# Kernel optimization log

Measured on AMD Instinct MI355X. Metric: run time of the kernel, lower is better.

Reference implementation:

```python
import jax, jax.numpy as jnp
import numpy as np

B, N, H, IN, OUT = 2, 4096, 64, 32, 8


def setup_inputs() -> dict:
    key = jax.random.key(0)
    ks = jax.random.split(key, 18)
    sc = 0.1  # xavier-ish scale for H=64
    mask = lambda k: (jax.random.uniform(k, (1, N, N)) < 0.1).astype(jnp.float32)
    return {
        "x0": jax.random.normal(ks[0], (B, N, IN), jnp.float32),
        "h0": jax.random.normal(ks[1], (B, N, H), jnp.float32),
        "h1": jax.random.normal(ks[2], (B, N, H), jnp.float32),
        "h2": jax.random.normal(ks[3], (B, N, H), jnp.float32),
        "m00": mask(ks[4]), "m20": mask(ks[5]), "m01": mask(ks[6]),
        "m11": mask(ks[7]), "m12": mask(ks[8]), "m22": mask(ks[9]),
        "Wq": jax.random.normal(ks[10], (3, H, H), jnp.float32) * sc,
        "Wk": jax.random.normal(ks[11], (6, H, H), jnp.float32) * sc,
        "Wsu0": jax.random.normal(ks[12], (H, IN + H), jnp.float32) * sc,
        "Wsu12": jax.random.normal(ks[13], (2, H, H), jnp.float32) * sc,
        "Wdt": jax.random.normal(ks[14], (3, H, H), jnp.float32) * sc,
        "bdt": jnp.zeros((3, H), jnp.float32),
        "step_size": jnp.array(1.0, jnp.float32),
        "out_scale": jnp.array(10.0, jnp.float32),
    }


def _cosine_acc(q, keys_and_masks_and_vals):
    # q: [B,N,H]; each entry: (keys [B,Np,H], mask [1,N,Np], vals [B,Np,H])
    qn = q / jnp.linalg.norm(q, axis=2, keepdims=True)
    acc = 0.0
    for k, m, v in keys_and_masks_and_vals:
        kn = k / jnp.linalg.norm(k, axis=2, keepdims=True)
        scale = 1.0 / jnp.sum(m, axis=2, keepdims=True)
        rel = scale * m * jnp.einsum("bnh,bmh->bnm", qn, kn)  # [B,N,Np]
        acc = acc + jnp.einsum("bnm,bmh->bnh", rel, v)
    return acc


def reference(x0, h0, h1, h2, m00, m20, m01, m11, m12, m22,
              Wq, Wk, Wsu0, Wsu12, Wdt, bdt, step_size, out_scale):
    # queries per successor type, keys per edge; edges (pred->succ):
    # 0->0 (k0), 2->0 (k1), 0->1 (k2), 1->1 (k3), 1->2 (k4), 2->2 (k5)
    q0 = h0 @ Wq[0].T
    q1 = h1 @ Wq[1].T
    q2 = h2 @ Wq[2].T
    acc0 = _cosine_acc(q0, [(h0 @ Wk[0].T, m00, h0), (h2 @ Wk[1].T, m20, h2)])
    acc1 = _cosine_acc(q1, [(h0 @ Wk[2].T, m01, h0), (h1 @ Wk[3].T, m11, h1)])
    acc2 = _cosine_acc(q2, [(h1 @ Wk[4].T, m12, h1), (h2 @ Wk[5].T, m22, h2)])

    def step(h, acc_in, Wsu, t):
        dt = 2.0 * jax.nn.sigmoid(h @ Wdt[t].T + bdt[t]) - 1.0
        return h + step_size * dt * (acc_in @ Wsu.T)

    h0n = step(h0, jnp.concatenate([x0, acc0], axis=2), Wsu0, 0)
    h1n = step(h1, acc1, Wsu12[0], 1)
    h2n = step(h2, acc2, Wsu12[1], 2)
    out2 = out_scale * h2n[:, :, :OUT]
    return (out2, h0n, h1n, h2n)
```

## Files before the change

kernel.cpp:

```cpp
#include <hip/hip_runtime.h>

typedef __bf16 bf16;
typedef bf16 bf16x8 __attribute__((ext_vector_type(8)));
typedef float f32x4 __attribute__((ext_vector_type(4)));
typedef unsigned int u32x4 __attribute__((ext_vector_type(4)));
typedef unsigned short u16x8 __attribute__((ext_vector_type(8)));
typedef unsigned int uint;

constexpr int NT = 4096;

__device__ __forceinline__ bf16x8 ld8f(const float* p) {
    f32x4 a = *(const f32x4*)p;
    f32x4 b = *(const f32x4*)(p + 4);
    bf16x8 v;
    v[0] = (bf16)a[0]; v[1] = (bf16)a[1]; v[2] = (bf16)a[2]; v[3] = (bf16)a[3];
    v[4] = (bf16)b[0]; v[5] = (bf16)b[1]; v[6] = (bf16)b[2]; v[7] = (bf16)b[3];
    return v;
}

__device__ __forceinline__ uint pack2(float a, float b) {
    unsigned short ua = __builtin_bit_cast(unsigned short, (bf16)a);
    unsigned short ub = __builtin_bit_cast(unsigned short, (bf16)b);
    return (uint)ua | ((uint)ub << 16);
}

__global__ __launch_bounds__(256) void prep_kernel(
    const float* __restrict__ h0, const float* __restrict__ h1, const float* __restrict__ h2,
    const float* __restrict__ Wq, const float* __restrict__ Wk,
    bf16* __restrict__ qn, bf16* __restrict__ kn, bf16* __restrict__ vT)
{
    __shared__ __align__(16) unsigned short tlds[4][16][72];
    const int tid = threadIdx.x, wid = tid >> 6, lane = tid & 63;
    const int l15 = lane & 15, quad = lane >> 4;
    const int bx = blockIdx.x;
    const int rt = bx & 127, sl = bx >> 7;
    const int g0 = rt * 64;
    const int grow = g0 + wid * 16 + l15;
    const float* hs[3] = {h0, h1, h2};

    bf16x8 af[3][2];
#pragma unroll
    for (int p = 0; p < 3; p++)
#pragma unroll
        for (int hc = 0; hc < 2; hc++)
            af[p][hc] = ld8f(hs[p] + (size_t)grow * 64 + hc * 32 + quad * 8);

    if (sl == 0) {
        const int gr0 = g0 + wid * 16;
        const int bb = gr0 >> 12, n0 = gr0 & 4095;
#pragma unroll
        for (int p = 0; p < 3; p++) {
#pragma unroll
            for (int hc = 0; hc < 2; hc++)
                *(u16x8*)(&tlds[wid][l15][hc * 32 + quad * 8]) = __builtin_bit_cast(u16x8, af[p][hc]);
            unsigned short vals[16];
#pragma unroll
            for (int r = 0; r < 16; r++) vals[r] = tlds[wid][r][lane];
            uint us[8];
#pragma unroll
            for (int k = 0; k < 8; k++) us[k] = (uint)vals[2 * k] | ((uint)vals[2 * k + 1] << 16);
            uint* dst = (uint*)(vT + ((size_t)(p * 2 + bb) * 64 + lane) * NT + n0);
            u32x4 w0 = {us[0], us[1], us[2], us[3]};
            u32x4 w1 = {us[4], us[5], us[6], us[7]};
            *(u32x4*)dst = w0;
            *(u32x4*)(dst + 4) = w1;
        }
    }

    const int predmap[6] = {0, 2, 0, 1, 1, 2};
    const int pj0 = sl * 3;
#pragma unroll
    for (int pi = 0; pi < 3; pi++) {
        const int pj = pj0 + pi;
        const float* W = (pj < 3) ? (Wq + pj * 4096) : (Wk + (pj - 3) * 4096);
        const int src = (pj < 3) ? pj : predmap[pj - 3];
        bf16* outp = (pj < 3) ? (qn + (size_t)pj * 2 * NT * 64)
                              : (kn + (size_t)(pj - 3) * 2 * NT * 64);
        f32x4 s[4];
#pragma unroll
        for (int it = 0; it < 4; it++) {
            f32x4 acc = {0.f, 0.f, 0.f, 0.f};
#pragma unroll
            for (int hc = 0; hc < 2; hc++) {
                bf16x8 wb = ld8f(W + (size_t)(it * 16 + l15) * 64 + hc * 32 + quad * 8);
                acc = __builtin_amdgcn_mfma_f32_16x16x32_bf16(af[src][hc], wb, acc, 0, 0, 0);
            }
            s[it] = acc;
        }
#pragma unroll
        for (int r = 0; r < 4; r++) {
            float ss = s[0][r] * s[0][r] + s[1][r] * s[1][r] + s[2][r] * s[2][r] + s[3][r] * s[3][r];
            ss += __shfl_xor(ss, 1); ss += __shfl_xor(ss, 2);
            ss += __shfl_xor(ss, 4); ss += __shfl_xor(ss, 8);
            float rn = rsqrtf(ss);
            s[0][r] *= rn; s[1][r] *= rn; s[2][r] *= rn; s[3][r] *= rn;
        }
        const int rowbase = g0 + wid * 16 + quad * 4;
#pragma unroll
        for (int it = 0; it < 4; it++)
#pragma unroll
            for (int r = 0; r < 4; r++)
                outp[(size_t)(rowbase + r) * 64 + it * 16 + l15] = (bf16)s[it][r];
    }
}

template<int JC>
__global__ __launch_bounds__(256, 3) void attn_kernel(
    const bf16* __restrict__ qn, const bf16* __restrict__ kn, const bf16* __restrict__ vT,
    const float* __restrict__ m00, const float* __restrict__ m20, const float* __restrict__ m01,
    const float* __restrict__ m11, const float* __restrict__ m12, const float* __restrict__ m22,
    float* __restrict__ Pacc, float* __restrict__ rsO)
{
    __shared__ __align__(16) bf16 Klds[2][64][72];
    __shared__ __align__(16) bf16 Vlds[2][64][72];
    const int tid = threadIdx.x, wid = tid >> 6, lane = tid & 63;
    const int l15 = lane & 15, quad = lane >> 4;
    const int bx = blockIdx.x;
    const int e = bx / (32 * JC);
    const int rem = bx % (32 * JC);
    const int qt = rem / JC, jcv = rem % JC;
    const int qrow0 = qt * 128, wstrip = wid * 32;
    const int qtypemap[6] = {0, 0, 1, 1, 2, 2};
    const int predmap[6]  = {0, 2, 0, 1, 1, 2};
    const float* masks[6] = {m00, m20, m01, m11, m12, m22};
    const float* __restrict__ mask = masks[e];
    const int qtv = qtypemap[e], pv = predmap[e];
    constexpr int JSPAN = NT / JC;
    const int jbeg = jcv * JSPAN, jend = jbeg + JSPAN;

    bf16x8 Qf[2][2][2];
#pragma unroll
    for (int b = 0; b < 2; b++)
#pragma unroll
        for (int mt = 0; mt < 2; mt++)
#pragma unroll
            for (int hc = 0; hc < 2; hc++)
                Qf[b][mt][hc] = *(const bf16x8*)(qn +
                    ((size_t)(qtv * 2 + b) * NT + qrow0 + wstrip + mt * 16 + l15) * 64 +
                    hc * 32 + quad * 8);

    f32x4 acc2[2][4][2];
#pragma unroll
    for (int b = 0; b < 2; b++)
#pragma unroll
        for (int ht = 0; ht < 4; ht++)
#pragma unroll
            for (int mt = 0; mt < 2; mt++) {
                f32x4 z = {0.f, 0.f, 0.f, 0.f};
                acc2[b][ht][mt] = z;
            }
    float rsl[2] = {0.f, 0.f};

#pragma unroll 1
    for (int j0 = jbeg; j0 < jend; j0 += 64) {
        __syncthreads();
#pragma unroll
        for (int i = 0; i < 4; i++) {
            int u = tid + 256 * i;
            int b = u >> 9, jl = (u >> 3) & 63, ch = u & 7;
            *(u32x4*)(&Klds[b][jl][ch * 8]) =
                *(const u32x4*)(kn + ((size_t)(e * 2 + b) * NT + j0 + jl) * 64 + ch * 8);
            *(u32x4*)(&Vlds[b][jl][ch * 8]) =
                *(const u32x4*)(vT + ((size_t)(pv * 2 + b) * 64 + jl) * NT + j0 + ch * 8);
        }
        __syncthreads();

        f32x4 mv[2][4];
#pragma unroll
        for (int mt = 0; mt < 2; mt++)
#pragma unroll
            for (int jt = 0; jt < 4; jt++) {
                mv[mt][jt] = *(const f32x4*)(mask +
                    (size_t)(qrow0 + wstrip + mt * 16 + l15) * NT + j0 + jt * 16 + quad * 4);
                rsl[mt] += mv[mt][jt][0] + mv[mt][jt][1] + mv[mt][jt][2] + mv[mt][jt][3];
            }

#pragma unroll
        for (int b = 0; b < 2; b++) {
            uint Pd[4][2][2];
#pragma unroll
            for (int jt = 0; jt < 4; jt++)
#pragma unroll
                for (int mt = 0; mt < 2; mt++) {
                    f32x4 sc = {0.f, 0.f, 0.f, 0.f};
#pragma unroll
                    for (int hc = 0; hc < 2; hc++) {
                        bf16x8 a = *(const bf16x8*)(&Klds[b][jt * 16 + l15][hc * 32 + quad * 8]);
                        sc = __builtin_amdgcn_mfma_f32_16x16x32_bf16(a, Qf[b][mt][hc], sc, 0, 0, 0);
                    }
                    sc[0] *= mv[mt][jt][0]; sc[1] *= mv[mt][jt][1];
                    sc[2] *= mv[mt][jt][2]; sc[3] *= mv[mt][jt][3];
                    Pd[jt][mt][0] = pack2(sc[0], sc[1]);
                    Pd[jt][mt][1] = pack2(sc[2], sc[3]);
                }

            uint Bf[2][2][4];
#pragma unroll
            for (int mt = 0; mt < 2; mt++)
#pragma unroll
                for (int c = 0; c < 2; c++)
#pragma unroll
                    for (int v = 0; v < 4; v++) {
                        int srclane = ((((quad & 1) * 2 + (v >> 1)) * 16 + l15) << 2);
                        int lo = __builtin_amdgcn_ds_bpermute(srclane, (int)Pd[2 * c][mt][v & 1]);
                        int hi = __builtin_amdgcn_ds_bpermute(srclane, (int)Pd[2 * c + 1][mt][v & 1]);
                        Bf[mt][c][v] = (quad & 2) ? (uint)hi : (uint)lo;
                    }

#pragma unroll
            for (int ht = 0; ht < 4; ht++)
#pragma unroll
                for (int c = 0; c < 2; c++) {
                    bf16x8 a = *(const bf16x8*)(&Vlds[b][ht * 16 + l15][c * 32 + quad * 8]);
#pragma unroll
                    for (int mt = 0; mt < 2; mt++) {
                        u32x4 t = {Bf[mt][c][0], Bf[mt][c][1], Bf[mt][c][2], Bf[mt][c][3]};
                        bf16x8 bbv = __builtin_bit_cast(bf16x8, t);
                        acc2[b][ht][mt] =
                            __builtin_amdgcn_mfma_f32_16x16x32_bf16(a, bbv, acc2[b][ht][mt], 0, 0, 0);
                    }
                }
        }
    }

#pragma unroll
    for (int b = 0; b < 2; b++)
#pragma unroll
        for (int ht = 0; ht < 4; ht++)
#pragma unroll
            for (int mt = 0; mt < 2; mt++) {
                int row = qrow0 + wstrip + mt * 16 + l15;
                *(f32x4*)(Pacc + (((size_t)(jcv * 6 + e) * 2 + b) * NT + row) * 64 +
                          ht * 16 + quad * 4) = acc2[b][ht][mt];
            }
#pragma unroll
    for (int mt = 0; mt < 2; mt++) {
        float v = rsl[mt];
        v += __shfl_xor(v, 16);
        v += __shfl_xor(v, 32);
        if (quad == 0)
            rsO[(size_t)(jcv * 6 + e) * NT + qrow0 + wstrip + mt * 16 + l15] = v;
    }
}

template<int JC>
__global__ __launch_bounds__(256) void update_kernel(
    const float* __restrict__ x0, const float* __restrict__ h0,
    const float* __restrict__ h1, const float* __restrict__ h2,
    const float* __restrict__ Wsu0, const float* __restrict__ Wsu12,
    const float* __restrict__ Wdt, const float* __restrict__ bdt,
    const float* __restrict__ stepp, const float* __restrict__ oscp,
    const float* __restrict__ Pacc, const float* __restrict__ rs,
    float* __restrict__ dout)
{
    const int tid = threadIdx.x, wid = tid >> 6, lane = tid & 63;
    const int l15 = lane & 15, quad = lane >> 4;
    const int bx = blockIdx.x;
    const int rt = bx & 127, t = bx >> 7;
    const int g0 = rt * 64;
    const int grow = g0 + wid * 16 + l15;
    const int n = grow & 4095, bb = grow >> 12;
    const float step = *stepp, osc = *oscp;
    const float* hs[3] = {h0, h1, h2};
    const float* __restrict__ ht_base = hs[t];

    bf16x8 afh[2], afacc[2], afx;
#pragma unroll
    for (int hc = 0; hc < 2; hc++)
        afh[hc] = ld8f(ht_base + (size_t)grow * 64 + hc * 32 + quad * 8);
    if (t == 0) afx = ld8f(x0 + (size_t)grow * 32 + quad * 8);

    float s0 = 0.f, s1 = 0.f;
#pragma unroll
    for (int jc = 0; jc < JC; jc++) {
        s0 += rs[(size_t)(jc * 6 + 2 * t) * NT + n];
        s1 += rs[(size_t)(jc * 6 + 2 * t + 1) * NT + n];
    }
    const float i0 = 1.f / s0, i1 = 1.f / s1;
#pragma unroll
    for (int hc = 0; hc < 2; hc++) {
        f32x4 A0 = {0.f,0.f,0.f,0.f}, A1 = {0.f,0.f,0.f,0.f};
        f32x4 B0 = {0.f,0.f,0.f,0.f}, B1 = {0.f,0.f,0.f,0.f};
#pragma unroll
        for (int jc = 0; jc < JC; jc++) {
            const float* p0 = Pacc + (((size_t)(jc * 6 + 2 * t) * 2 + bb) * NT + n) * 64 + hc * 32 + quad * 8;
            const float* p1 = Pacc + (((size_t)(jc * 6 + 2 * t + 1) * 2 + bb) * NT + n) * 64 + hc * 32 + quad * 8;
            A0 += *(const f32x4*)p0;       A1 += *(const f32x4*)(p0 + 4);
            B0 += *(const f32x4*)p1;       B1 += *(const f32x4*)(p1 + 4);
        }
        bf16x8 v;
        v[0] = (bf16)(A0[0] * i0 + B0[0] * i1);
        v[1] = (bf16)(A0[1] * i0 + B0[1] * i1);
        v[2] = (bf16)(A0[2] * i0 + B0[2] * i1);
        v[3] = (bf16)(A0[3] * i0 + B0[3] * i1);
        v[4] = (bf16)(A1[0] * i0 + B1[0] * i1);
        v[5] = (bf16)(A1[1] * i0 + B1[1] * i1);
        v[6] = (bf16)(A1[2] * i0 + B1[2] * i1);
        v[7] = (bf16)(A1[3] * i0 + B1[3] * i1);
        afacc[hc] = v;
    }

    float bdtv[4];
#pragma unroll
    for (int it = 0; it < 4; it++)
        bdtv[it] = bdt[t * 64 + it * 16 + l15];

#pragma unroll
    for (int it = 0; it < 4; it++) {
        f32x4 z = {0.f, 0.f, 0.f, 0.f};
        f32x4 u = {0.f, 0.f, 0.f, 0.f};
#pragma unroll
        for (int hc = 0; hc < 2; hc++) {
            bf16x8 wb = ld8f(Wdt + (size_t)t * 4096 + (size_t)(it * 16 + l15) * 64 + hc * 32 + quad * 8);
            z = __builtin_amdgcn_mfma_f32_16x16x32_bf16(afh[hc], wb, z, 0, 0, 0);
        }
        if (t == 0) {
            bf16x8 w0 = ld8f(Wsu0 + (size_t)(it * 16 + l15) * 96 + quad * 8);
            u = __builtin_amdgcn_mfma_f32_16x16x32_bf16(afx, w0, u, 0, 0, 0);
#pragma unroll
            for (int kc = 0; kc < 2; kc++) {
                bf16x8 wk = ld8f(Wsu0 + (size_t)(it * 16 + l15) * 96 + 32 + kc * 32 + quad * 8);
                u = __builtin_amdgcn_mfma_f32_16x16x32_bf16(afacc[kc], wk, u, 0, 0, 0);
            }
        } else {
#pragma unroll
            for (int kc = 0; kc < 2; kc++) {
                bf16x8 wk = ld8f(Wsu12 + (size_t)(t - 1) * 4096 + (size_t)(it * 16 + l15) * 64 + kc * 32 + quad * 8);
                u = __builtin_amdgcn_mfma_f32_16x16x32_bf16(afacc[kc], wk, u, 0, 0, 0);
            }
        }
        const int colg = it * 16 + l15;
#pragma unroll
        for (int r = 0; r < 4; r++) {
            int row = g0 + wid * 16 + quad * 4 + r;
            float zz = z[r] + bdtv[it];
            float dtv = 2.f / (1.f + __expf(-zz)) - 1.f;
            float hval = ht_base[(size_t)row * 64 + colg];
            float hn = hval + step * dtv * u[r];
            dout[65536 + (size_t)t * 524288 + (size_t)row * 64 + colg] = hn;
            if (t == 2 && colg < 8)
                dout[(size_t)row * 8 + colg] = osc * hn;
        }
    }
}

extern "C" void kernel_launch(void* const* d_in, const int* in_sizes, int n_in,
                              void* d_out, int out_size, void* d_ws, size_t ws_size,
                              hipStream_t stream) {
    const float* x0   = (const float*)d_in[0];
    const float* h0   = (const float*)d_in[1];
    const float* h1   = (const float*)d_in[2];
    const float* h2   = (const float*)d_in[3];
    const float* m00  = (const float*)d_in[4];
    const float* m20  = (const float*)d_in[5];
    const float* m01  = (const float*)d_in[6];
    const float* m11  = (const float*)d_in[7];
    const float* m12  = (const float*)d_in[8];
    const float* m22  = (const float*)d_in[9];
    const float* Wq   = (const float*)d_in[10];
    const float* Wk   = (const float*)d_in[11];
    const float* Wsu0 = (const float*)d_in[12];
    const float* Wsu12= (const float*)d_in[13];
    const float* Wdt  = (const float*)d_in[14];
    const float* bdt  = (const float*)d_in[15];
    const float* step = (const float*)d_in[16];
    const float* oscl = (const float*)d_in[17];

    bf16* qn  = (bf16*)d_ws;
    bf16* kn  = qn + 1572864;
    bf16* vT  = kn + 3145728;
    float* Pacc = (float*)(vT + 1572864);

    auto need = [](size_t jc) { return 12582912 + jc * 12582912 + jc * 98304; };
    const int JC = (ws_size >= need(4)) ? 4 : ((ws_size >= need(2)) ? 2 : 1);

    prep_kernel<<<384, 256, 0, stream>>>(h0, h1, h2, Wq, Wk, qn, kn, vT);

    if (JC == 4) {
        float* rs = Pacc + (size_t)4 * 3145728;
        attn_kernel<4><<<192 * 4, 256, 0, stream>>>(qn, kn, vT, m00, m20, m01, m11, m12, m22, Pacc, rs);
        update_kernel<4><<<384, 256, 0, stream>>>(x0, h0, h1, h2, Wsu0, Wsu12, Wdt, bdt,
                                                  step, oscl, Pacc, rs, (float*)d_out);
    } else if (JC == 2) {
        float* rs = Pacc + (size_t)2 * 3145728;
        attn_kernel<2><<<192 * 2, 256, 0, stream>>>(qn, kn, vT, m00, m20, m01, m11, m12, m22, Pacc, rs);
        update_kernel<2><<<384, 256, 0, stream>>>(x0, h0, h1, h2, Wsu0, Wsu12, Wdt, bdt,
                                                  step, oscl, Pacc, rs, (float*)d_out);
    } else {
        float* rs = Pacc + (size_t)1 * 3145728;
        attn_kernel<1><<<192, 256, 0, stream>>>(qn, kn, vT, m00, m20, m01, m11, m12, m22, Pacc, rs);
        update_kernel<1><<<384, 256, 0, stream>>>(x0, h0, h1, h2, Wsu0, Wsu12, Wdt, bdt,
                                                  step, oscl, Pacc, rs, (float*)d_out);
    }
}
```

Baseline: 519.8 us.

## Drop LDS staging in attention, shrink query tile, store partials as bf16, raise split

The attention kernel no longer stages K and V tiles through shared memory or uses block barriers. Each wave now handles one 16-row query strip and reads K and V fragments straight from global memory or cache. The query tile shrinks from 128 to 64 rows, the key split factor rises to 8, and occupancy hint goes to 5, giving more blocks and more parallelism. Partial accumulators are written as bf16 instead of fp32, halving the partial-sum traffic at some precision cost. In exchange, K/V reuse across waves is lost, so redundant global loads increase.

```diff
diff --git a/kernel.cpp b/kernel.cpp
--- a/kernel.cpp
+++ b/kernel.cpp
@@ -3,9 +3,10 @@
 typedef __bf16 bf16;
 typedef bf16 bf16x8 __attribute__((ext_vector_type(8)));
 typedef float f32x4 __attribute__((ext_vector_type(4)));
-typedef unsigned int u32x4 __attribute__((ext_vector_type(4)));
+typedef unsigned int uint;
+typedef uint u32x2 __attribute__((ext_vector_type(2)));
+typedef uint u32x4 __attribute__((ext_vector_type(4)));
 typedef unsigned short u16x8 __attribute__((ext_vector_type(8)));
-typedef unsigned int uint;
 
 constexpr int NT = 4096;
 
@@ -105,120 +106,100 @@
 }
 
 template<int JC>
-__global__ __launch_bounds__(256, 3) void attn_kernel(
+__global__ __launch_bounds__(256, 5) void attn_kernel(
     const bf16* __restrict__ qn, const bf16* __restrict__ kn, const bf16* __restrict__ vT,
     const float* __restrict__ m00, const float* __restrict__ m20, const float* __restrict__ m01,
     const float* __restrict__ m11, const float* __restrict__ m12, const float* __restrict__ m22,
-    float* __restrict__ Pacc, float* __restrict__ rsO)
+    bf16* __restrict__ Pacc, float* __restrict__ rsO)
 {
-    __shared__ __align__(16) bf16 Klds[2][64][72];
-    __shared__ __align__(16) bf16 Vlds[2][64][72];
     const int tid = threadIdx.x, wid = tid >> 6, lane = tid & 63;
     const int l15 = lane & 15, quad = lane >> 4;
     const int bx = blockIdx.x;
-    const int e = bx / (32 * JC);
-    const int rem = bx % (32 * JC);
+    const int e = bx / (64 * JC);
+    const int rem = bx % (64 * JC);
     const int qt = rem / JC, jcv = rem % JC;
-    const int qrow0 = qt * 128, wstrip = wid * 32;
+    const int qrow = qt * 64 + wid * 16 + l15;
     const int qtypemap[6] = {0, 0, 1, 1, 2, 2};
     const int predmap[6]  = {0, 2, 0, 1, 1, 2};
     const float* masks[6] = {m00, m20, m01, m11, m12, m22};
     const float* __restrict__ mask = masks[e];
     const int qtv = qtypemap[e], pv = predmap[e];
     constexpr int JSPAN = NT / JC;
-    const int jbeg = jcv * JSPAN, jend = jbeg + JSPAN;
-
-    bf16x8 Qf[2][2][2];
+    const int jbeg = jcv * JSPAN;
+
+    bf16x8 Qf[2][2];
 #pragma unroll
     for (int b = 0; b < 2; b++)
 #pragma unroll
-        for (int mt = 0; mt < 2; mt++)
-#pragma unroll
-            for (int hc = 0; hc < 2; hc++)
-                Qf[b][mt][hc] = *(const bf16x8*)(qn +
-                    ((size_t)(qtv * 2 + b) * NT + qrow0 + wstrip + mt * 16 + l15) * 64 +
-                    hc * 32 + quad * 8);
-
-    f32x4 acc2[2][4][2];
+        for (int hc = 0; hc < 2; hc++)
+            Qf[b][hc] = *(const bf16x8*)(qn +
+                ((size_t)(qtv * 2 + b) * NT + qrow) * 64 + hc * 32 + quad * 8);
+
+    f32x4 acc2[2][4];
 #pragma unroll
     for (int b = 0; b < 2; b++)
 #pragma unroll
-        for (int ht = 0; ht < 4; ht++)
-#pragma unroll
-            for (int mt = 0; mt < 2; mt++) {
-                f32x4 z = {0.f, 0.f, 0.f, 0.f};
-                acc2[b][ht][mt] = z;
+        for (int ht = 0; ht < 4; ht++) {
+            f32x4 z = {0.f, 0.f, 0.f, 0.f};
+            acc2[b][ht] = z;
+        }
+    float rsl = 0.f;
+    const size_t mrow = (size_t)qrow * NT;
+    const size_t kb0 = (size_t)(e * 2) * NT * 64;
+
+#pragma unroll 1
+    for (int ji = 0; ji < JSPAN / 64; ji++) {
+        const int j0 = jbeg + ji * 64;
+
+        f32x4 mv[4];
+#pragma unroll
+        for (int jt = 0; jt < 4; jt++)
+            mv[jt] = *(const f32x4*)(mask + mrow + j0 + jt * 16 + quad * 4);
+#pragma unroll
+        for (int jt = 0; jt < 4; jt++)
+            rsl += mv[jt][0] + mv[jt][1] + mv[jt][2] + mv[jt][3];
+
+        uint Pd[2][4][2];
+#pragma unroll
+        for (int jt = 0; jt < 4; jt++)
+#pragma unroll
+            for (int b = 0; b < 2; b++) {
+                f32x4 sc = {0.f, 0.f, 0.f, 0.f};
+#pragma unroll
+                for (int hc = 0; hc < 2; hc++) {
+                    bf16x8 ka = *(const bf16x8*)(kn + kb0 +
+                        ((size_t)b * NT + j0 + jt * 16 + l15) * 64 + hc * 32 + quad * 8);
+                    sc = __builtin_amdgcn_mfma_f32_16x16x32_bf16(ka, Qf[b][hc], sc, 0, 0, 0);
+                }
+                sc[0] *= mv[jt][0]; sc[1] *= mv[jt][1];
+                sc[2] *= mv[jt][2]; sc[3] *= mv[jt][3];
+                Pd[b][jt][0] = pack2(sc[0], sc[1]);
+                Pd[b][jt][1] = pack2(sc[2], sc[3]);
             }
-    float rsl[2] = {0.f, 0.f};
-
-#pragma unroll 1
-    for (int j0 = jbeg; j0 < jend; j0 += 64) {
-        __syncthreads();
-#pragma unroll
-        for (int i = 0; i < 4; i++) {
-            int u = tid + 256 * i;
-            int b = u >> 9, jl = (u >> 3) & 63, ch = u & 7;
-            *(u32x4*)(&Klds[b][jl][ch * 8]) =
-                *(const u32x4*)(kn + ((size_t)(e * 2 + b) * NT + j0 + jl) * 64 + ch * 8);
-            *(u32x4*)(&Vlds[b][jl][ch * 8]) =
-                *(const u32x4*)(vT + ((size_t)(pv * 2 + b) * 64 + jl) * NT + j0 + ch * 8);
-        }
-        __syncthreads();
-
-        f32x4 mv[2][4];
-#pragma unroll
-        for (int mt = 0; mt < 2; mt++)
-#pragma unroll
-            for (int jt = 0; jt < 4; jt++) {
-                mv[mt][jt] = *(const f32x4*)(mask +
-                    (size_t)(qrow0 + wstrip + mt * 16 + l15) * NT + j0 + jt * 16 + quad * 4);
-                rsl[mt] += mv[mt][jt][0] + mv[mt][jt][1] + mv[mt][jt][2] + mv[mt][jt][3];
-            }
 
 #pragma unroll
         for (int b = 0; b < 2; b++) {
-            uint Pd[4][2][2];
-#pragma unroll
-            for (int jt = 0; jt < 4; jt++)
-#pragma unroll
-                for (int mt = 0; mt < 2; mt++) {
-                    f32x4 sc = {0.f, 0.f, 0.f, 0.f};
-#pragma unroll
-                    for (int hc = 0; hc < 2; hc++) {
-                        bf16x8 a = *(const bf16x8*)(&Klds[b][jt * 16 + l15][hc * 32 + quad * 8]);
-                        sc = __builtin_amdgcn_mfma_f32_16x16x32_bf16(a, Qf[b][mt][hc], sc, 0, 0, 0);
-                    }
-                    sc[0] *= mv[mt][jt][0]; sc[1] *= mv[mt][jt][1];
-                    sc[2] *= mv[mt][jt][2]; sc[3] *= mv[mt][jt][3];
-                    Pd[jt][mt][0] = pack2(sc[0], sc[1]);
-                    Pd[jt][mt][1] = pack2(sc[2], sc[3]);
+            uint Bf[2][4];
+#pragma unroll
+            for (int c = 0; c < 2; c++)
+#pragma unroll
+                for (int v = 0; v < 4; v++) {
+                    int srclane = ((((quad & 1) * 2 + (v >> 1)) * 16 + l15) << 2);
+                    int lo = __builtin_amdgcn_ds_bpermute(srclane, (int)Pd[b][2 * c][v & 1]);
+                    int hi = __builtin_amdgcn_ds_bpermute(srclane, (int)Pd[b][2 * c + 1][v & 1]);
+                    Bf[c][v] = (quad & 2) ? (uint)hi : (uint)lo;
                 }
 
-            uint Bf[2][2][4];
-#pragma unroll
-            for (int mt = 0; mt < 2; mt++)
-#pragma unroll
-                for (int c = 0; c < 2; c++)
-#pragma unroll
-                    for (int v = 0; v < 4; v++) {
-                        int srclane = ((((quad & 1) * 2 + (v >> 1)) * 16 + l15) << 2);
-                        int lo = __builtin_amdgcn_ds_bpermute(srclane, (int)Pd[2 * c][mt][v & 1]);
-                        int hi = __builtin_amdgcn_ds_bpermute(srclane, (int)Pd[2 * c + 1][mt][v & 1]);
-                        Bf[mt][c][v] = (quad & 2) ? (uint)hi : (uint)lo;
-                    }
-
 #pragma unroll
             for (int ht = 0; ht < 4; ht++)
 #pragma unroll
                 for (int c = 0; c < 2; c++) {
-                    bf16x8 a = *(const bf16x8*)(&Vlds[b][ht * 16 + l15][c * 32 + quad * 8]);
-#pragma unroll
-                    for (int mt = 0; mt < 2; mt++) {
-                        u32x4 t = {Bf[mt][c][0], Bf[mt][c][1], Bf[mt][c][2], Bf[mt][c][3]};
-                        bf16x8 bbv = __builtin_bit_cast(bf16x8, t);
-                        acc2[b][ht][mt] =
-                            __builtin_amdgcn_mfma_f32_16x16x32_bf16(a, bbv, acc2[b][ht][mt], 0, 0, 0);
-                    }
+                    bf16x8 av = *(const bf16x8*)(vT +
+                        ((size_t)((pv * 2 + b) * 64 + ht * 16 + l15)) * NT + j0 + c * 32 + quad * 8);
+                    u32x4 t = {Bf[c][0], Bf[c][1], Bf[c][2], Bf[c][3]};
+                    bf16x8 bbv = __builtin_bit_cast(bf16x8, t);
+                    acc2[b][ht] =
+                        __builtin_amdgcn_mfma_f32_16x16x32_bf16(av, bbv, acc2[b][ht], 0, 0, 0);
                 }
         }
     }
@@ -226,20 +207,19 @@
 #pragma unroll
     for (int b = 0; b < 2; b++)
 #pragma unroll
-        for (int ht = 0; ht < 4; ht++)
-#pragma unroll
-            for (int mt = 0; mt < 2; mt++) {
-                int row = qrow0 + wstrip + mt * 16 + l15;
-                *(f32x4*)(Pacc + (((size_t)(jcv * 6 + e) * 2 + b) * NT + row) * 64 +
-                          ht * 16 + quad * 4) = acc2[b][ht][mt];
-            }
-#pragma unroll
-    for (int mt = 0; mt < 2; mt++) {
-        float v = rsl[mt];
+        for (int ht = 0; ht < 4; ht++) {
+            u32x2 pk;
+            pk[0] = pack2(acc2[b][ht][0], acc2[b][ht][1]);
+            pk[1] = pack2(acc2[b][ht][2], acc2[b][ht][3]);
+            *(u32x2*)(Pacc + (((size_t)(jcv * 6 + e) * 2 + b) * NT + qrow) * 64 +
+                      ht * 16 + quad * 4) = pk;
+        }
+    {
+        float v = rsl;
         v += __shfl_xor(v, 16);
         v += __shfl_xor(v, 32);
         if (quad == 0)
-            rsO[(size_t)(jcv * 6 + e) * NT + qrow0 + wstrip + mt * 16 + l15] = v;
+            rsO[(size_t)(jcv * 6 + e) * NT + qrow] = v;
     }
 }
 
@@ -250,7 +230,7 @@
     const float* __restrict__ Wsu0, const float* __restrict__ Wsu12,
     const float* __restrict__ Wdt, const float* __restrict__ bdt,
     const float* __restrict__ stepp, const float* __restrict__ oscp,
-    const float* __restrict__ Pacc, const float* __restrict__ rs,
+    const bf16* __restrict__ Pacc, const float* __restrict__ rs,
     float* __restrict__ dout)
 {
     const int tid = threadIdx.x, wid = tid >> 6, lane = tid & 63;
@@ -279,24 +259,19 @@
     const float i0 = 1.f / s0, i1 = 1.f / s1;
 #pragma unroll
     for (int hc = 0; hc < 2; hc++) {
-        f32x4 A0 = {0.f,0.f,0.f,0.f}, A1 = {0.f,0.f,0.f,0.f};
-        f32x4 B0 = {0.f,0.f,0.f,0.f}, B1 = {0.f,0.f,0.f,0.f};
+        float A[8] = {0,0,0,0,0,0,0,0}, Bv[8] = {0,0,0,0,0,0,0,0};
 #pragma unroll
         for (int jc = 0; jc < JC; jc++) {
-            const float* p0 = Pacc + (((size_t)(jc * 6 + 2 * t) * 2 + bb) * NT + n) * 64 + hc * 32 + quad * 8;
-            const float* p1 = Pacc + (((size_t)(jc * 6 + 2 * t + 1) * 2 + bb) * NT + n) * 64 + hc * 32 + quad * 8;
-            A0 += *(const f32x4*)p0;       A1 += *(const f32x4*)(p0 + 4);
-            B0 += *(const f32x4*)p1;       B1 += *(const f32x4*)(p1 + 4);
+            bf16x8 a = *(const bf16x8*)(Pacc +
+                (((size_t)(jc * 6 + 2 * t) * 2 + bb) * NT + n) * 64 + hc * 32 + quad * 8);
+            bf16x8 c = *(const bf16x8*)(Pacc +
+                (((size_t)(jc * 6 + 2 * t + 1) * 2 + bb) * NT + n) * 64 + hc * 32 + quad * 8);
+#pragma unroll
+            for (int i = 0; i < 8; i++) { A[i] += (float)a[i]; Bv[i] += (float)c[i]; }
         }
         bf16x8 v;
-        v[0] = (bf16)(A0[0] * i0 + B0[0] * i1);
-        v[1] = (bf16)(A0[1] * i0 + B0[1] * i1);
-        v[2] = (bf16)(A0[2] * i0 + B0[2] * i1);
-        v[3] = (bf16)(A0[3] * i0 + B0[3] * i1);
-        v[4] = (bf16)(A1[0] * i0 + B1[0] * i1);
-        v[5] = (bf16)(A1[1] * i0 + B1[1] * i1);
-        v[6] = (bf16)(A1[2] * i0 + B1[2] * i1);
-        v[7] = (bf16)(A1[3] * i0 + B1[3] * i1);
+#pragma unroll
+        for (int i = 0; i < 8; i++) v[i] = (bf16)(A[i] * i0 + Bv[i] * i1);
         afacc[hc] = v;
     }
 
@@ -369,27 +344,27 @@
     bf16* qn  = (bf16*)d_ws;
     bf16* kn  = qn + 1572864;
     bf16* vT  = kn + 3145728;
-    float* Pacc = (float*)(vT + 1572864);
-
-    auto need = [](size_t jc) { return 12582912 + jc * 12582912 + jc * 98304; };
-    const int JC = (ws_size >= need(4)) ? 4 : ((ws_size >= need(2)) ? 2 : 1);
+    bf16* Pacc = vT + 1572864;
+
+    auto need = [](size_t jc) { return 12582912 + jc * 6291456 + jc * 98304; };
+    const int JC = (ws_size >= need(8)) ? 8 : ((ws_size >= need(4)) ? 4 : 2);
 
     prep_kernel<<<384, 256, 0, stream>>>(h0, h1, h2, Wq, Wk, qn, kn, vT);
 
-    if (JC == 4) {
-        float* rs = Pacc + (size_t)4 * 3145728;
-        attn_kernel<4><<<192 * 4, 256, 0, stream>>>(qn, kn, vT, m00, m20, m01, m11, m12, m22, Pacc, rs);
+    if (JC == 8) {
+        float* rs = (float*)(Pacc + (size_t)8 * 3145728);
+        attn_kernel<8><<<6 * 64 * 8, 256, 0, stream>>>(qn, kn, vT, m00, m20, m01, m11, m12, m22, Pacc, rs);
+        update_kernel<8><<<384, 256, 0, stream>>>(x0, h0, h1, h2, Wsu0, Wsu12, Wdt, bdt,
+                                                  step, oscl, Pacc, rs, (float*)d_out);
+    } else if (JC == 4) {
+        float* rs = (float*)(Pacc + (size_t)4 * 3145728);
+        attn_kernel<4><<<6 * 64 * 4, 256, 0, stream>>>(qn, kn, vT, m00, m20, m01, m11, m12, m22, Pacc, rs);
         update_kernel<4><<<384, 256, 0, stream>>>(x0, h0, h1, h2, Wsu0, Wsu12, Wdt, bdt,
                                                   step, oscl, Pacc, rs, (float*)d_out);
-    } else if (JC == 2) {
-        float* rs = Pacc + (size_t)2 * 3145728;
-        attn_kernel<2><<<192 * 2, 256, 0, stream>>>(qn, kn, vT, m00, m20, m01, m11, m12, m22, Pacc, rs);
+    } else {
+        float* rs = (float*)(Pacc + (size_t)2 * 3145728);
+        attn_kernel<2><<<6 * 64 * 2, 256, 0, stream>>>(qn, kn, vT, m00, m20, m01, m11, m12, m22, Pacc, rs);
         update_kernel<2><<<384, 256, 0, stream>>>(x0, h0, h1, h2, Wsu0, Wsu12, Wdt, bdt,
                                                   step, oscl, Pacc, rs, (float*)d_out);
-    } else {
-        float* rs = Pacc + (size_t)1 * 3145728;
-        attn_kernel<1><<<192, 256, 0, stream>>>(qn, kn, vT, m00, m20, m01, m11, m12, m22, Pacc, rs);
-        update_kernel<1><<<384, 256, 0, stream>>>(x0, h0, h1, h2, Wsu0, Wsu12, Wdt, bdt,
-                                                  step, oscl, Pacc, rs, (float*)d_out);
-    }
-}
+    }
+}
```

After: 917.2 us. 1.76x slower.

## Prefetch next K/V tile and mask into registers during attention compute

Applied to the files above, without the earlier changes.

The attention loop now loads the next 64-column K, V and mask tile into registers while the current tile is being processed, so global loads overlap with MFMA work rather than stalling right after each barrier. The score computation for both batches is done before the PV stage, which allows the mask prefetch to be issued in between. The Pacc partial-accumulator layout is also transposed to [h][n], giving scalar coalesced stores in attention and strided scalar loads in update. The cost is higher register pressure from kreg/vreg/mv and a redundant prefetch on the last iteration.

```diff
diff --git a/kernel.cpp b/kernel.cpp
--- a/kernel.cpp
+++ b/kernel.cpp
@@ -3,9 +3,9 @@
 typedef __bf16 bf16;
 typedef bf16 bf16x8 __attribute__((ext_vector_type(8)));
 typedef float f32x4 __attribute__((ext_vector_type(4)));
-typedef unsigned int u32x4 __attribute__((ext_vector_type(4)));
+typedef unsigned int uint;
+typedef uint u32x4 __attribute__((ext_vector_type(4)));
 typedef unsigned short u16x8 __attribute__((ext_vector_type(8)));
-typedef unsigned int uint;
 
 constexpr int NT = 4096;
 
@@ -126,7 +126,15 @@
     const float* __restrict__ mask = masks[e];
     const int qtv = qtypemap[e], pv = predmap[e];
     constexpr int JSPAN = NT / JC;
-    const int jbeg = jcv * JSPAN, jend = jbeg + JSPAN;
+    constexpr int NI = JSPAN / 64;
+    const int jbeg = jcv * JSPAN;
+
+    int s_b[4], s_jl[4], s_ch[4];
+#pragma unroll
+    for (int i = 0; i < 4; i++) {
+        int u = tid + 256 * i;
+        s_b[i] = u >> 9; s_jl[i] = (u >> 3) & 63; s_ch[i] = u & 7;
+    }
 
     bf16x8 Qf[2][2][2];
 #pragma unroll
@@ -151,35 +159,49 @@
             }
     float rsl[2] = {0.f, 0.f};
 
+    u32x4 kreg[4], vreg[4];
+#pragma unroll
+    for (int i = 0; i < 4; i++) {
+        kreg[i] = *(const u32x4*)(kn + ((size_t)(e * 2 + s_b[i]) * NT + jbeg + s_jl[i]) * 64 + s_ch[i] * 8);
+        vreg[i] = *(const u32x4*)(vT + ((size_t)(pv * 2 + s_b[i]) * 64 + s_jl[i]) * NT + jbeg + s_ch[i] * 8);
+    }
+    f32x4 mv[2][4];
+#pragma unroll
+    for (int mt = 0; mt < 2; mt++)
+#pragma unroll
+        for (int jt = 0; jt < 4; jt++)
+            mv[mt][jt] = *(const f32x4*)(mask +
+                (size_t)(qrow0 + wstrip + mt * 16 + l15) * NT + jbeg + jt * 16 + quad * 4);
+
 #pragma unroll 1
-    for (int j0 = jbeg; j0 < jend; j0 += 64) {
+    for (int ji = 0; ji < NI; ji++) {
+        const int jn = (ji + 1 < NI) ? (jbeg + (ji + 1) * 64) : jbeg;
+
         __syncthreads();
 #pragma unroll
         for (int i = 0; i < 4; i++) {
-            int u = tid + 256 * i;
-            int b = u >> 9, jl = (u >> 3) & 63, ch = u & 7;
-            *(u32x4*)(&Klds[b][jl][ch * 8]) =
-                *(const u32x4*)(kn + ((size_t)(e * 2 + b) * NT + j0 + jl) * 64 + ch * 8);
-            *(u32x4*)(&Vlds[b][jl][ch * 8]) =
-                *(const u32x4*)(vT + ((size_t)(pv * 2 + b) * 64 + jl) * NT + j0 + ch * 8);
+            *(u32x4*)(&Klds[s_b[i]][s_jl[i]][s_ch[i] * 8]) = kreg[i];
+            *(u32x4*)(&Vlds[s_b[i]][s_jl[i]][s_ch[i] * 8]) = vreg[i];
         }
         __syncthreads();
 
-        f32x4 mv[2][4];
+#pragma unroll
+        for (int i = 0; i < 4; i++) {
+            kreg[i] = *(const u32x4*)(kn + ((size_t)(e * 2 + s_b[i]) * NT + jn + s_jl[i]) * 64 + s_ch[i] * 8);
+            vreg[i] = *(const u32x4*)(vT + ((size_t)(pv * 2 + s_b[i]) * 64 + s_jl[i]) * NT + jn + s_ch[i] * 8);
+        }
+
 #pragma unroll
         for (int mt = 0; mt < 2; mt++)
 #pragma unroll
-            for (int jt = 0; jt < 4; jt++) {
-                mv[mt][jt] = *(const f32x4*)(mask +
-                    (size_t)(qrow0 + wstrip + mt * 16 + l15) * NT + j0 + jt * 16 + quad * 4);
+            for (int jt = 0; jt < 4; jt++)
                 rsl[mt] += mv[mt][jt][0] + mv[mt][jt][1] + mv[mt][jt][2] + mv[mt][jt][3];
-            }
-
-#pragma unroll
-        for (int b = 0; b < 2; b++) {
-            uint Pd[4][2][2];
-#pragma unroll
-            for (int jt = 0; jt < 4; jt++)
+
+        uint Pd[2][4][2][2];
+#pragma unroll
+        for (int jt = 0; jt < 4; jt++)
+#pragma unroll
+            for (int b = 0; b < 2; b++)
 #pragma unroll
                 for (int mt = 0; mt < 2; mt++) {
                     f32x4 sc = {0.f, 0.f, 0.f, 0.f};
@@ -190,10 +212,19 @@
                     }
                     sc[0] *= mv[mt][jt][0]; sc[1] *= mv[mt][jt][1];
                     sc[2] *= mv[mt][jt][2]; sc[3] *= mv[mt][jt][3];
-                    Pd[jt][mt][0] = pack2(sc[0], sc[1]);
-                    Pd[jt][mt][1] = pack2(sc[2], sc[3]);
+                    Pd[b][jt][mt][0] = pack2(sc[0], sc[1]);
+                    Pd[b][jt][mt][1] = pack2(sc[2], sc[3]);
                 }
 
+#pragma unroll
+        for (int mt = 0; mt < 2; mt++)
+#pragma unroll
+            for (int jt = 0; jt < 4; jt++)
+                mv[mt][jt] = *(const f32x4*)(mask +
+                    (size_t)(qrow0 + wstrip + mt * 16 + l15) * NT + jn + jt * 16 + quad * 4);
+
+#pragma unroll
+        for (int b = 0; b < 2; b++) {
             uint Bf[2][2][4];
 #pragma unroll
             for (int mt = 0; mt < 2; mt++)
@@ -202,11 +233,10 @@
 #pragma unroll
                     for (int v = 0; v < 4; v++) {
                         int srclane = ((((quad & 1) * 2 + (v >> 1)) * 16 + l15) << 2);
-                        int lo = __builtin_amdgcn_ds_bpermute(srclane, (int)Pd[2 * c][mt][v & 1]);
-                        int hi = __builtin_amdgcn_ds_bpermute(srclane, (int)Pd[2 * c + 1][mt][v & 1]);
+                        int lo = __builtin_amdgcn_ds_bpermute(srclane, (int)Pd[b][2 * c][mt][v & 1]);
+                        int hi = __builtin_amdgcn_ds_bpermute(srclane, (int)Pd[b][2 * c + 1][mt][v & 1]);
                         Bf[mt][c][v] = (quad & 2) ? (uint)hi : (uint)lo;
                     }
-
 #pragma unroll
             for (int ht = 0; ht < 4; ht++)
 #pragma unroll
@@ -229,9 +259,12 @@
         for (int ht = 0; ht < 4; ht++)
 #pragma unroll
             for (int mt = 0; mt < 2; mt++) {
-                int row = qrow0 + wstrip + mt * 16 + l15;
-                *(f32x4*)(Pacc + (((size_t)(jcv * 6 + e) * 2 + b) * NT + row) * 64 +
-                          ht * 16 + quad * 4) = acc2[b][ht][mt];
+                const int n = qrow0 + wstrip + mt * 16 + l15;
+#pragma unroll
+                for (int r = 0; r < 4; r++) {
+                    const int h = ht * 16 + quad * 4 + r;
+                    Pacc[(((size_t)(jcv * 6 + e) * 2 + b) * 64 + h) * NT + n] = acc2[b][ht][mt][r];
+                }
             }
 #pragma unroll
     for (int mt = 0; mt < 2; mt++) {
@@ -279,24 +312,21 @@
     const float i0 = 1.f / s0, i1 = 1.f / s1;
 #pragma unroll
     for (int hc = 0; hc < 2; hc++) {
-        f32x4 A0 = {0.f,0.f,0.f,0.f}, A1 = {0.f,0.f,0.f,0.f};
-        f32x4 B0 = {0.f,0.f,0.f,0.f}, B1 = {0.f,0.f,0.f,0.f};
+        float S0[8] = {0,0,0,0,0,0,0,0}, S1[8] = {0,0,0,0,0,0,0,0};
 #pragma unroll
         for (int jc = 0; jc < JC; jc++) {
-            const float* p0 = Pacc + (((size_t)(jc * 6 + 2 * t) * 2 + bb) * NT + n) * 64 + hc * 32 + quad * 8;
-            const float* p1 = Pacc + (((size_t)(jc * 6 + 2 * t + 1) * 2 + bb) * NT + n) * 64 + hc * 32 + quad * 8;
-            A0 += *(const f32x4*)p0;       A1 += *(const f32x4*)(p0 + 4);
-            B0 += *(const f32x4*)p1;       B1 += *(const f32x4*)(p1 + 4);
+            const float* b0 = Pacc + (((size_t)(jc * 6 + 2 * t) * 2 + bb) * 64) * NT + n;
+            const float* b1 = Pacc + (((size_t)(jc * 6 + 2 * t + 1) * 2 + bb) * 64) * NT + n;
+#pragma unroll
+            for (int j = 0; j < 8; j++) {
+                const int h = hc * 32 + quad * 8 + j;
+                S0[j] += b0[(size_t)h * NT];
+                S1[j] += b1[(size_t)h * NT];
+            }
         }
         bf16x8 v;
-        v[0] = (bf16)(A0[0] * i0 + B0[0] * i1);
-        v[1] = (bf16)(A0[1] * i0 + B0[1] * i1);
-        v[2] = (bf16)(A0[2] * i0 + B0[2] * i1);
-        v[3] = (bf16)(A0[3] * i0 + B0[3] * i1);
-        v[4] = (bf16)(A1[0] * i0 + B1[0] * i1);
-        v[5] = (bf16)(A1[1] * i0 + B1[1] * i1);
-        v[6] = (bf16)(A1[2] * i0 + B1[2] * i1);
-        v[7] = (bf16)(A1[3] * i0 + B1[3] * i1);
+#pragma unroll
+        for (int j = 0; j < 8; j++) v[j] = (bf16)(S0[j] * i0 + S1[j] * i1);
         afacc[hc] = v;
     }
 
@@ -378,17 +408,17 @@
 
     if (JC == 4) {
         float* rs = Pacc + (size_t)4 * 3145728;
-        attn_kernel<4><<<192 * 4, 256, 0, stream>>>(qn, kn, vT, m00, m20, m01, m11, m12, m22, Pacc, rs);
+        attn_kernel<4><<<6 * 32 * 4, 256, 0, stream>>>(qn, kn, vT, m00, m20, m01, m11, m12, m22, Pacc, rs);
         update_kernel<4><<<384, 256, 0, stream>>>(x0, h0, h1, h2, Wsu0, Wsu12, Wdt, bdt,
                                                   step, oscl, Pacc, rs, (float*)d_out);
     } else if (JC == 2) {
         float* rs = Pacc + (size_t)2 * 3145728;
-        attn_kernel<2><<<192 * 2, 256, 0, stream>>>(qn, kn, vT, m00, m20, m01, m11, m12, m22, Pacc, rs);
+        attn_kernel<2><<<6 * 32 * 2, 256, 0, stream>>>(qn, kn, vT, m00, m20, m01, m11, m12, m22, Pacc, rs);
         update_kernel<2><<<384, 256, 0, stream>>>(x0, h0, h1, h2, Wsu0, Wsu12, Wdt, bdt,
                                                   step, oscl, Pacc, rs, (float*)d_out);
     } else {
         float* rs = Pacc + (size_t)1 * 3145728;
-        attn_kernel<1><<<192, 256, 0, stream>>>(qn, kn, vT, m00, m20, m01, m11, m12, m22, Pacc, rs);
+        attn_kernel<1><<<6 * 32 * 1, 256, 0, stream>>>(qn, kn, vT, m00, m20, m01, m11, m12, m22, Pacc, rs);
         update_kernel<1><<<384, 256, 0, stream>>>(x0, h0, h1, h2, Wsu0, Wsu12, Wdt, bdt,
                                                   step, oscl, Pacc, rs, (float*)d_out);
     }
```

Result: faster. 494.0 us (-5.0%).
